# Performance work log

Hardware: AMD Instinct MI355X
Metric: run time of the kernel (lower is better)

## Reference

```python
import jax, jax.numpy as jnp
import numpy as np

S, B, H, E = 2048, 4, 1024, 8
FF = 4 * H


def openai_gelu(x):
    # Megatron's tanh-approx gelu: 0.5*x*(1+tanh(sqrt(2/pi)*x*(1+0.044715*x^2)))
    return 0.5 * x * (1.0 + jnp.tanh(0.7978845608028654 * x * (1.0 + 0.044715 * x * x)))


def setup_inputs() -> dict:
    key = jax.random.key(0)
    ks = jax.random.split(key, 6)
    hidden_states = jax.random.normal(ks[0], (S, B, H), dtype=jnp.float32)
    # router: nn.Linear(H, E) with bias -> weight [E, H], bias [E]
    router_w = jax.random.normal(ks[1], (E, H), dtype=jnp.float32) / np.sqrt(H)
    router_b = jnp.zeros((E,), dtype=jnp.float32)
    # per-expert MLP weights, stacked on leading expert axis (torch Linear weight = [out, in])
    w1 = jax.random.normal(ks[2], (E, FF, H), dtype=jnp.float32) * np.sqrt(2.0 / (H + FF))
    b1 = jnp.zeros((E, FF), dtype=jnp.float32)
    w2 = jax.random.normal(ks[3], (E, H, FF), dtype=jnp.float32) * np.sqrt(2.0 / (H + FF))
    b2 = jnp.zeros((E, H), dtype=jnp.float32)
    return {"hidden_states": hidden_states, "router_w": router_w, "router_b": router_b,
            "w1": w1, "b1": b1, "w2": w2, "b2": b2}


def reference(hidden_states, router_w, router_b, w1, b1, w2, b2):
    s, b, h = hidden_states.shape
    e = w1.shape[0]
    # router + top-1 selection
    route = jax.nn.softmax(hidden_states @ router_w.T + router_b, axis=2)  # [s,b,E]
    max_prob = jnp.max(route, axis=2).reshape(-1, 1)                       # [N,1]
    max_ind = jnp.argmax(route, axis=2).reshape(-1)                        # [N]
    x = hidden_states.reshape(-1, h)                                       # [N,h]
    out = jnp.zeros_like(x)
    out_bias = jnp.zeros_like(x)
    # E is small and fixed; top-1 routing covers every token exactly once.
    for ei in range(e):
        inter = openai_gelu(x @ w1[ei].T + b1[ei])   # [N, 4h]
        y = inter @ w2[ei].T                          # [N, h]
        mask = (max_ind == ei)[:, None]
        out = jnp.where(mask, y, out)
        out_bias = jnp.where(mask, b2[ei][None, :], out_bias)
    out = (out * max_prob).reshape(s, b, h)
    out_bias = (out_bias * max_prob).reshape(s, b, h)
    return (out, out_bias)
```

## Files before the change

### kernel.cpp

```cpp
#include <hip/hip_runtime.h>
#include <math.h>

typedef float  f32x4  __attribute__((ext_vector_type(4)));
typedef short  bf16x8 __attribute__((ext_vector_type(8)));

#define NTOK 8192
#define H    1024
#define FF   4096
#define NEXP 8
#define MAXT128 72

__device__ __forceinline__ unsigned short f2bf(float f) {
    unsigned int u = __float_as_uint(f);
    u += 0x7fffu + ((u >> 16) & 1u);
    return (unsigned short)(u >> 16);
}

__device__ __forceinline__ void gload16(const void* g, void* l) {
    __builtin_amdgcn_global_load_lds((const __attribute__((address_space(1))) void*)g,
                                     (__attribute__((address_space(3))) void*)l, 16, 0, 0);
}

__global__ void __launch_bounds__(256)
router_k(const float* __restrict__ x, const float* __restrict__ rw, const float* __restrict__ rb,
         float* __restrict__ maxp, int* __restrict__ maxi, int* __restrict__ counts) {
    const int lane = threadIdx.x & 63;
    const int t = blockIdx.x * 4 + (threadIdx.x >> 6);
    const float4* xr = (const float4*)(x + (size_t)t * H);
    float acc[NEXP];
#pragma unroll
    for (int e = 0; e < NEXP; ++e) acc[e] = 0.f;
#pragma unroll
    for (int c = 0; c < 4; ++c) {
        float4 xv = xr[lane + 64 * c];
#pragma unroll
        for (int e = 0; e < NEXP; ++e) {
            float4 wv = ((const float4*)(rw + e * H))[lane + 64 * c];
            acc[e] += xv.x * wv.x + xv.y * wv.y + xv.z * wv.z + xv.w * wv.w;
        }
    }
#pragma unroll
    for (int e = 0; e < NEXP; ++e) {
#pragma unroll
        for (int off = 32; off > 0; off >>= 1) acc[e] += __shfl_xor(acc[e], off);
    }
    if (lane == 0) {
        float best = -1e30f; int bi = 0;
#pragma unroll
        for (int e = 0; e < NEXP; ++e) {
            float v = acc[e] + rb[e];
            acc[e] = v;
            if (v > best) { best = v; bi = e; }
        }
        float s = 0.f;
#pragma unroll
        for (int e = 0; e < NEXP; ++e) s += __expf(acc[e] - best);
        maxp[t] = 1.0f / s;
        maxi[t] = bi;
        atomicAdd(&counts[bi * 32], 1);
    }
}

__global__ void scan_k(const int* __restrict__ counts, int* __restrict__ offs,
                       int* __restrict__ tile_e, int* __restrict__ tile_r0, int* __restrict__ ntiles) {
    int off = 0, ti = 0;
    for (int e = 0; e < NEXP; ++e) {
        offs[e] = off;
        int nt = (counts[e * 32] + 127) >> 7;
        for (int j = 0; j < nt; ++j) { tile_e[ti] = e; tile_r0[ti] = off + (j << 7); ++ti; }
        off += nt << 7;
    }
    offs[NEXP] = off;
    *ntiles = ti;
}

__global__ void __launch_bounds__(256)
gather_k(const float* __restrict__ x, const int* __restrict__ maxi, const int* __restrict__ offs,
         int* __restrict__ cursor, int* __restrict__ perm, unsigned short* __restrict__ ab) {
    const int lane = threadIdx.x & 63;
    const int t = blockIdx.x * 4 + (threadIdx.x >> 6);
    int pos = 0;
    if (lane == 0) {
        int e = maxi[t];
        pos = offs[e] + atomicAdd(&cursor[e * 32], 1);
        perm[pos] = t;
    }
    pos = __shfl(pos, 0);
    const float4* xr = (const float4*)(x + (size_t)t * H);
    ushort4* ar = (ushort4*)(ab + (size_t)pos * H);
#pragma unroll
    for (int c = 0; c < 4; ++c) {
        float4 v = xr[lane + 64 * c];
        ar[lane + 64 * c] = make_ushort4(f2bf(v.x), f2bf(v.y), f2bf(v.z), f2bf(v.w));
    }
}

__global__ void __launch_bounds__(256)
cvt_k(const float4* __restrict__ w1, const float4* __restrict__ w2,
      ushort4* __restrict__ d1, ushort4* __restrict__ d2, int n4) {
    const int stride = gridDim.x * blockDim.x;
    for (int i = blockIdx.x * blockDim.x + threadIdx.x; i < n4; i += stride) {
        float4 v = w1[i]; d1[i] = make_ushort4(f2bf(v.x), f2bf(v.y), f2bf(v.z), f2bf(v.w));
        float4 u = w2[i]; d2[i] = make_ushort4(f2bf(u.x), f2bf(u.y), f2bf(u.z), f2bf(u.w));
    }
}

template<int KB>
__device__ __forceinline__ void gemm_core(const char* Ag, const char* Bg,
                                          unsigned short* As, unsigned short* Bs,
                                          f32x4 (&acc)[4][4]) {
    const int tid  = threadIdx.x;
    const int lane = tid & 63;
    const int wv   = tid >> 6;
    const int wr   = wv >> 1, wc = wv & 1;

    int goff[4];
#pragma unroll
    for (int c = 0; c < 4; ++c) {
        int op = c * 4096 + wv * 1024 + lane * 16;
        int ol = op ^ (((op >> 7) & 7) << 4);
        goff[c] = (ol >> 7) * KB + (ol & 127);
    }
    const int rA  = (wr * 64 + (lane & 15)) * 128;
    const int rB  = (wc * 64 + (lane & 15)) * 128;
    const int xr  = (lane & 7) << 4;
    const int cb0 = (lane >> 4) << 4;

#pragma unroll 1
    for (int kt = 0; kt < KB / 128; ++kt) {
        const int kb = kt * 128;
#pragma unroll
        for (int c = 0; c < 4; ++c)
            gload16(Ag + goff[c] + kb, (char*)As + c * 4096 + wv * 1024);
#pragma unroll
        for (int c = 0; c < 4; ++c)
            gload16(Bg + goff[c] + kb, (char*)Bs + c * 4096 + wv * 1024);
        __syncthreads();
#pragma unroll
        for (int kk = 0; kk < 2; ++kk) {
            bf16x8 a[4], b[4];
            const int cb = kk * 64 + cb0;
#pragma unroll
            for (int m = 0; m < 4; ++m)
                a[m] = *(const bf16x8*)((const char*)As + ((rA + m * 2048 + cb) ^ xr));
#pragma unroll
            for (int n = 0; n < 4; ++n)
                b[n] = *(const bf16x8*)((const char*)Bs + ((rB + n * 2048 + cb) ^ xr));
#pragma unroll
            for (int m = 0; m < 4; ++m)
#pragma unroll
                for (int n = 0; n < 4; ++n)
                    asm volatile("v_mfma_f32_16x16x32_bf16 %0, %1, %2, %0"
                                 : "+v"(acc[m][n]) : "v"(a[m]), "v"(b[n]));
        }
        __syncthreads();
    }
}

__global__ void __launch_bounds__(256)
gemm1_k(const unsigned short* __restrict__ ab, const unsigned short* __restrict__ w1b,
        const float* __restrict__ b1, unsigned short* __restrict__ inter,
        const int* __restrict__ tile_e, const int* __restrict__ tile_r0,
        const int* __restrict__ ntiles) {
    if ((int)blockIdx.y >= *ntiles) return;
    __shared__ alignas(16) unsigned short As[128 * 64];
    __shared__ alignas(16) unsigned short Bs[128 * 64];
    const int e    = tile_e[blockIdx.y];
    const int row0 = tile_r0[blockIdx.y];
    const int f0   = blockIdx.x * 128;
    f32x4 acc[4][4];
#pragma unroll
    for (int m = 0; m < 4; ++m)
#pragma unroll
        for (int n = 0; n < 4; ++n)
#pragma unroll
            for (int j = 0; j < 4; ++j) acc[m][n][j] = 0.f;

    gemm_core<2 * H>((const char*)(ab + (size_t)row0 * H),
                     (const char*)(w1b + ((size_t)e * FF + f0) * H), As, Bs, acc);

    const int lane = threadIdx.x & 63;
    const int wv = threadIdx.x >> 6, wr = wv >> 1, wc = wv & 1;
    const int lr = (lane >> 4) << 2, lc = lane & 15;
#pragma unroll
    for (int n = 0; n < 4; ++n) {
        const int gcol = f0 + wc * 64 + n * 16 + lc;
        const float bias = b1[e * FF + gcol];
#pragma unroll
        for (int m = 0; m < 4; ++m) {
            const int gr0 = row0 + wr * 64 + m * 16 + lr;
#pragma unroll
            for (int r = 0; r < 4; ++r) {
                float v = acc[m][n][r] + bias;
                float ex = __expf(1.5957691216057308f * v * (1.0f + 0.044715f * v * v));
                float u  = v - v / (ex + 1.0f);
                inter[(size_t)(gr0 + r) * FF + gcol] = f2bf(u);
            }
        }
    }
}

__global__ void __launch_bounds__(256)
gemm2_k(const unsigned short* __restrict__ inter, const unsigned short* __restrict__ w2b,
        float* __restrict__ out,
        const int* __restrict__ tile_e, const int* __restrict__ tile_r0, const int* __restrict__ ntiles,
        const int* __restrict__ counts, const int* __restrict__ offs,
        const int* __restrict__ perm, const float* __restrict__ maxp) {
    if ((int)blockIdx.y >= *ntiles) return;
    __shared__ alignas(16) unsigned short As[128 * 64];
    __shared__ alignas(16) unsigned short Bs[128 * 64];
    const int e    = tile_e[blockIdx.y];
    const int row0 = tile_r0[blockIdx.y];
    const int h0   = blockIdx.x * 128;
    f32x4 acc[4][4];
#pragma unroll
    for (int m = 0; m < 4; ++m)
#pragma unroll
        for (int n = 0; n < 4; ++n)
#pragma unroll
            for (int j = 0; j < 4; ++j) acc[m][n][j] = 0.f;

    gemm_core<2 * FF>((const char*)(inter + (size_t)row0 * FF),
                      (const char*)(w2b + ((size_t)e * H + h0) * FF), As, Bs, acc);

    const int lane = threadIdx.x & 63;
    const int wv = threadIdx.x >> 6, wr = wv >> 1, wc = wv & 1;
    const int lr = (lane >> 4) << 2, lc = lane & 15;
    const int cnt = counts[e * 32], offe = offs[e];
#pragma unroll
    for (int m = 0; m < 4; ++m) {
#pragma unroll
        for (int r = 0; r < 4; ++r) {
            const int grow = row0 + wr * 64 + m * 16 + lr + r;
            if (grow - offe < cnt) {
                const int t = perm[grow];
                const float p = maxp[t];
#pragma unroll
                for (int n = 0; n < 4; ++n)
                    out[(size_t)t * H + h0 + wc * 64 + n * 16 + lc] = acc[m][n][r] * p;
            }
        }
    }
}

__global__ void __launch_bounds__(256)
bias_k(const float* __restrict__ b2, const int* __restrict__ maxi, const float* __restrict__ maxp,
       float* __restrict__ outb) {
    const int t = blockIdx.x;
    const int c = threadIdx.x;
    const int e = maxi[t];
    const float p = maxp[t];
    float4 v = ((const float4*)(b2 + e * H))[c];
    float4 r; r.x = v.x * p; r.y = v.y * p; r.z = v.z * p; r.w = v.w * p;
    ((float4*)(outb + (size_t)t * H))[c] = r;
}

extern "C" void kernel_launch(void* const* d_in, const int* in_sizes, int n_in,
                              void* d_out, int out_size, void* d_ws, size_t ws_size,
                              hipStream_t stream) {
    const float* x  = (const float*)d_in[0];
    const float* rw = (const float*)d_in[1];
    const float* rb = (const float*)d_in[2];
    const float* w1 = (const float*)d_in[3];
    const float* b1 = (const float*)d_in[4];
    const float* w2 = (const float*)d_in[5];
    const float* b2 = (const float*)d_in[6];
    float* out  = (float*)d_out;
    float* outb = out + (size_t)NTOK * H;

    char* ws = (char*)d_ws;
    unsigned short* W1B   = (unsigned short*)(ws);
    unsigned short* W2B   = (unsigned short*)(ws + 67108864);
    unsigned short* AB    = (unsigned short*)(ws + 134217728);
    unsigned short* INTER = (unsigned short*)(ws + 153092096);
    float* MAXP    = (float*)(ws + 228589568);
    int*   MAXI    = (int*)  (ws + 228622336);
    int*   PERM    = (int*)  (ws + 228655104);
    int*   COUNTS  = (int*)  (ws + 228691968);
    int*   CURSOR  = (int*)  (ws + 228692992);
    int*   OFFS    = (int*)  (ws + 228694016);
    int*   TILE_E  = (int*)  (ws + 228694080);
    int*   TILE_R0 = (int*)  (ws + 228694592);
    int*   NTILES  = (int*)  (ws + 228695104);

    (void)hipMemsetAsync(COUNTS, 0, 2048, stream);

    router_k<<<NTOK / 4, 256, 0, stream>>>(x, rw, rb, MAXP, MAXI, COUNTS);
    scan_k<<<1, 1, 0, stream>>>(COUNTS, OFFS, TILE_E, TILE_R0, NTILES);
    gather_k<<<NTOK / 4, 256, 0, stream>>>(x, MAXI, OFFS, CURSOR, PERM, AB);
    cvt_k<<<4096, 256, 0, stream>>>((const float4*)w1, (const float4*)w2,
                                    (ushort4*)W1B, (ushort4*)W2B, NEXP * FF * H / 4);
    gemm1_k<<<dim3(FF / 128, MAXT128), 256, 0, stream>>>(AB, W1B, b1, INTER,
                                                         TILE_E, TILE_R0, NTILES);
    gemm2_k<<<dim3(H / 128, MAXT128), 256, 0, stream>>>(INTER, W2B, out, TILE_E, TILE_R0, NTILES,
                                                        COUNTS, OFFS, PERM, MAXP);
    bias_k<<<NTOK, 256, 0, stream>>>(b2, MAXI, MAXP, outb);
}
```

Baseline: 350.8 us.

## Convert w2 in idle gemm1 blocks and fuse bias output into gemm2

The fp32-to-bf16 conversion of w2 moves out of the standalone conversion kernel. It now runs inside the gemm1 blocks that have no expert tile to process, so it overlaps with the first expert GEMM. The separate bias kernel is removed, and gemm2's epilogue writes the scaled b2 bias output next to the main output. This saves a launch and a pass over token indices. The risk is that the w2 conversion depends on how many gemm1 blocks are idle: only a few blocks may do it, which could leave a long tail, and if no blocks are idle it is skipped entirely.

```diff
diff --git a/kernel.cpp b/kernel.cpp
--- a/kernel.cpp
+++ b/kernel.cpp
@@ -96,12 +96,10 @@
 }
 
 __global__ void __launch_bounds__(256)
-cvt_k(const float4* __restrict__ w1, const float4* __restrict__ w2,
-      ushort4* __restrict__ d1, ushort4* __restrict__ d2, int n4) {
+cvt_k(const float4* __restrict__ w1, ushort4* __restrict__ d1, int n4) {
     const int stride = gridDim.x * blockDim.x;
     for (int i = blockIdx.x * blockDim.x + threadIdx.x; i < n4; i += stride) {
         float4 v = w1[i]; d1[i] = make_ushort4(f2bf(v.x), f2bf(v.y), f2bf(v.z), f2bf(v.w));
-        float4 u = w2[i]; d2[i] = make_ushort4(f2bf(u.x), f2bf(u.y), f2bf(u.z), f2bf(u.w));
     }
 }
 
@@ -161,8 +159,19 @@
 gemm1_k(const unsigned short* __restrict__ ab, const unsigned short* __restrict__ w1b,
         const float* __restrict__ b1, unsigned short* __restrict__ inter,
         const int* __restrict__ tile_e, const int* __restrict__ tile_r0,
-        const int* __restrict__ ntiles) {
-    if ((int)blockIdx.y >= *ntiles) return;
+        const int* __restrict__ ntiles,
+        const float4* __restrict__ w2f, ushort4* __restrict__ w2b4) {
+    const int nt = *ntiles;
+    if ((int)blockIdx.y >= nt) {
+        const int idle = ((int)gridDim.y - nt) * (int)gridDim.x;
+        const int wk   = ((int)blockIdx.y - nt) * (int)gridDim.x + (int)blockIdx.x;
+        const int n4   = NEXP * FF * H / 4;
+        for (int i = wk * 256 + (int)threadIdx.x; i < n4; i += idle * 256) {
+            float4 u = w2f[i];
+            w2b4[i] = make_ushort4(f2bf(u.x), f2bf(u.y), f2bf(u.z), f2bf(u.w));
+        }
+        return;
+    }
     __shared__ alignas(16) unsigned short As[128 * 64];
     __shared__ alignas(16) unsigned short Bs[128 * 64];
     const int e    = tile_e[blockIdx.y];
@@ -202,7 +211,7 @@
 
 __global__ void __launch_bounds__(256)
 gemm2_k(const unsigned short* __restrict__ inter, const unsigned short* __restrict__ w2b,
-        float* __restrict__ out,
+        const float* __restrict__ b2, float* __restrict__ out, float* __restrict__ outb,
         const int* __restrict__ tile_e, const int* __restrict__ tile_r0, const int* __restrict__ ntiles,
         const int* __restrict__ counts, const int* __restrict__ offs,
         const int* __restrict__ perm, const float* __restrict__ maxp) {
@@ -236,23 +245,14 @@
                 const int t = perm[grow];
                 const float p = maxp[t];
 #pragma unroll
-                for (int n = 0; n < 4; ++n)
-                    out[(size_t)t * H + h0 + wc * 64 + n * 16 + lc] = acc[m][n][r] * p;
+                for (int n = 0; n < 4; ++n) {
+                    const int col = h0 + wc * 64 + n * 16 + lc;
+                    out [(size_t)t * H + col] = acc[m][n][r] * p;
+                    outb[(size_t)t * H + col] = b2[e * H + col] * p;
+                }
             }
         }
     }
-}
-
-__global__ void __launch_bounds__(256)
-bias_k(const float* __restrict__ b2, const int* __restrict__ maxi, const float* __restrict__ maxp,
-       float* __restrict__ outb) {
-    const int t = blockIdx.x;
-    const int c = threadIdx.x;
-    const int e = maxi[t];
-    const float p = maxp[t];
-    float4 v = ((const float4*)(b2 + e * H))[c];
-    float4 r; r.x = v.x * p; r.y = v.y * p; r.z = v.z * p; r.w = v.w * p;
-    ((float4*)(outb + (size_t)t * H))[c] = r;
 }
 
 extern "C" void kernel_launch(void* const* d_in, const int* in_sizes, int n_in,
@@ -288,11 +288,11 @@
     router_k<<<NTOK / 4, 256, 0, stream>>>(x, rw, rb, MAXP, MAXI, COUNTS);
     scan_k<<<1, 1, 0, stream>>>(COUNTS, OFFS, TILE_E, TILE_R0, NTILES);
     gather_k<<<NTOK / 4, 256, 0, stream>>>(x, MAXI, OFFS, CURSOR, PERM, AB);
-    cvt_k<<<4096, 256, 0, stream>>>((const float4*)w1, (const float4*)w2,
-                                    (ushort4*)W1B, (ushort4*)W2B, NEXP * FF * H / 4);
+    cvt_k<<<4096, 256, 0, stream>>>((const float4*)w1, (ushort4*)W1B, NEXP * FF * H / 4);
     gemm1_k<<<dim3(FF / 128, MAXT128), 256, 0, stream>>>(AB, W1B, b1, INTER,
-                                                         TILE_E, TILE_R0, NTILES);
-    gemm2_k<<<dim3(H / 128, MAXT128), 256, 0, stream>>>(INTER, W2B, out, TILE_E, TILE_R0, NTILES,
+                                                         TILE_E, TILE_R0, NTILES,
+                                                         (const float4*)w2, (ushort4*)W2B);
+    gemm2_k<<<dim3(H / 128, MAXT128), 256, 0, stream>>>(INTER, W2B, b2, out, outb,
+                                                        TILE_E, TILE_R0, NTILES,
                                                         COUNTS, OFFS, PERM, MAXP);
-    bias_k<<<NTOK, 256, 0, stream>>>(b2, MAXI, MAXP, outb);
-}
+}
```

Measured after the change: 478.4 us. 36.4% more time.
